# Kernel tuning notes

Measured on AMD Instinct MI355X. Metric: run time of the kernel, lower is better.

Reference implementation:

```python
import jax, jax.numpy as jnp
import numpy as np
from jax import lax

CL, IL = 128, 64            # context_length, inst_length (globals in original)
PC, CH1, CH2, CH3 = 64, 128, 256, 256
CK1 = CK2 = CK3 = 3
F1, OUT = 400, 1
B = 4096
C3_OUT = CH3 * (CL - 1 - CK1 - CK2 - CK3 + 3)   # 256*121 = 30976
F1_IN = C3_OUT + CL * IL                        # 39168


def _uni(k, shape, fan_in):
    s = 1.0 / np.sqrt(fan_in)
    return jax.random.uniform(k, shape, jnp.float32, -s, s)


def setup_inputs() -> dict:
    key = jax.random.key(0)
    ks = jax.random.split(key, 14)
    x = jax.random.normal(ks[0], (B, CL * IL), jnp.float32)
    Wp = _uni(ks[1], (PC, IL, 2), IL * 2); bp = _uni(ks[2], (PC,), IL * 2)
    W1 = _uni(ks[3], (CH1, PC, CK1), PC * CK1); b1 = _uni(ks[4], (CH1,), PC * CK1)
    W2 = _uni(ks[5], (CH2, CH1, CK2), CH1 * CK2); b2 = _uni(ks[6], (CH2,), CH1 * CK2)
    W3 = _uni(ks[7], (CH3, CH2, CK3), CH2 * CK3); b3 = _uni(ks[8], (CH3,), CH2 * CK3)
    Wf1 = _uni(ks[9], (F1, F1_IN), F1_IN); bf1 = _uni(ks[10], (F1,), F1_IN)
    Wf2 = _uni(ks[11], (OUT, F1), F1); bf2 = _uni(ks[12], (OUT,), F1)
    return dict(x=x, Wp=Wp, bp=bp, W1=W1, b1=b1, W2=W2, b2=b2,
                W3=W3, b3=b3, Wf1=Wf1, bf1=bf1, Wf2=Wf2, bf2=bf2)


def _conv1d(h, w, b):
    # h: [B,C,L], w: [O,C,K], valid conv, stride 1
    return lax.conv_general_dilated(h, w, (1,), 'VALID',
                                    dimension_numbers=('NCH', 'OIH', 'NCH')) + b[None, :, None]


def reference(x, Wp, bp, W1, b1, W2, b2, W3, b3, Wf1, bf1, Wf2, bf2):
    b = x.shape[0]
    xt = x.reshape(b, CL, IL).transpose(0, 2, 1)          # [B, IL, CL]
    # Fused pairwise convp: original loops i=1..CL-1 over k=2 Conv1d on
    # (x[:,:,0], x[:,:,i]); equivalent to one shared term + one batched matmul.
    base = jnp.einsum('pc,bc->bp', Wp[:, :, 0], xt[:, :, 0])        # [B, PC]
    rest = jnp.einsum('pc,bci->bpi', Wp[:, :, 1], xt[:, :, 1:])     # [B, PC, CL-1]
    h = jax.nn.relu(base[:, :, None] + rest + bp[None, :, None])
    h = jax.nn.relu(_conv1d(h, W1, b1))
    h = jax.nn.relu(_conv1d(h, W2, b2))
    h = jax.nn.relu(_conv1d(h, W3, b3))
    h = h.reshape(b, C3_OUT)
    h = jnp.concatenate([h, xt.reshape(b, IL * CL)], axis=1)        # [B, F1_IN]
    h = jax.nn.relu(h @ Wf1.T + bf1)
    return h @ Wf2.T + bf2
```

## Files before the change

### kernel.cpp

```cpp
#include <hip/hip_runtime.h>


typedef __attribute__((ext_vector_type(8))) short bf16x8;
typedef __attribute__((ext_vector_type(4))) float f32x4;
typedef __attribute__((ext_vector_type(8))) unsigned short u16x8;
typedef __attribute__((ext_vector_type(4))) unsigned short u16x4;
typedef __attribute__((ext_vector_type(2))) unsigned int u32x2;
typedef __attribute__((ext_vector_type(4))) unsigned int u32x4;

#define DEVINL __device__ __forceinline__

DEVINL unsigned short f2bf(float f) {
  unsigned u = __builtin_bit_cast(unsigned, f);
  return (unsigned short)((u + 0x7fffu + ((u >> 16) & 1u)) >> 16);
}
DEVINL float bf2f(unsigned short h) {
  return __builtin_bit_cast(float, ((unsigned)h) << 16);
}
DEVINL unsigned cvtpk(float lo, float hi) {
  unsigned r;
  asm("v_cvt_pk_bf16_f32 %0, %1, %2" : "=v"(r) : "v"(lo), "v"(hi));
  return r;
}
DEVINL f32x4 mfma16(bf16x8 a, bf16x8 b, f32x4 c) {
  return __builtin_amdgcn_mfma_f32_16x16x32_bf16(a, b, c, 0, 0, 0);
}
DEVINL float relu(float v) { return v > 0.f ? v : 0.f; }
DEVINL int sxg(int r, int c, int sh) {
  return (r << sh) + (((c >> 3) ^ (r & 7)) << 3) + (c & 7);
}

constexpr int NB = 4096;

__global__ __launch_bounds__(256) void k_prep_w(
    const float* __restrict__ Wp, const float* __restrict__ W1,
    const float* __restrict__ W2, const float* __restrict__ W3,
    unsigned short* __restrict__ wp1r, unsigned short* __restrict__ wp0r,
    unsigned short* __restrict__ w1p, unsigned short* __restrict__ w2p,
    unsigned short* __restrict__ w3p) {
  int idx = blockIdx.x * 256 + threadIdx.x;
  if (idx < 4096) {
    int p = idx >> 6, i = idx & 63;
    wp1r[p * 64 + i] = f2bf(Wp[(p * 64 + i) * 2 + 1]);
    wp0r[i * 64 + p] = f2bf(Wp[(p * 64 + i) * 2 + 0]);
    return;
  }
  idx -= 4096;
  if (idx < 24576) {
    int f = idx >> 9, l = (idx >> 3) & 63, e = idx & 7;
    int mt = f & 7, t = f >> 3, ks = t & 1, k = t >> 1;
    int o = mt * 16 + (l & 15), c = ks * 32 + (l >> 4) * 8 + e;
    w1p[idx] = f2bf(W1[(o * 64 + c) * 3 + k]);
    return;
  }
  idx -= 24576;
  if (idx < 98304) {
    int f = idx >> 9, l = (idx >> 3) & 63, e = idx & 7;
    int mt = f & 15, t = f >> 4, ks = t & 3, k = t >> 2;
    int o = mt * 16 + (l & 15), c = ks * 32 + (l >> 4) * 8 + e;
    w2p[idx] = f2bf(W2[(o * 128 + c) * 3 + k]);
    return;
  }
  idx -= 98304;
  if (idx < 196608) {
    int f = idx >> 9, l = (idx >> 3) & 63, e = idx & 7;
    int mt = f & 15, t = f >> 4, ks = t & 7, k = t >> 3;
    int o = mt * 16 + (l & 15), c = ks * 32 + (l >> 4) * 8 + e;
    w3p[idx] = f2bf(W3[(o * 256 + c) * 3 + k]);
  }
}

__global__ __launch_bounds__(256) void k_prep_wf1(const float* __restrict__ wf1,
                                                  unsigned short* __restrict__ wf1r) {
  extern __shared__ unsigned short tls[];
  const int m = blockIdx.x / 5, q = blockIdx.x % 5, tid = threadIdx.x;
  unsigned short* dst = wf1r + (size_t)m * 39168;
  if (q < 4) {
    const float* src = wf1 + (size_t)m * 39168 + q * 7744;
    for (int idx = tid; idx < 7744; idx += 256) {
      int o = idx / 121, l = idx - o * 121;
      tls[o * 132 + l] = f2bf(src[idx]);
    }
    __syncthreads();
    for (int idx = tid; idx < 7744; idx += 256) {
      int l = idx >> 6, o = idx & 63;
      dst[l * 256 + q * 64 + o] = tls[o * 132 + l];
    }
  } else {
    const float* src = wf1 + (size_t)m * 39168 + 30976;
    for (int idx = tid; idx < 8192; idx += 256) {
      int il = idx >> 7, cl = idx & 127;
      tls[cl * 66 + il] = f2bf(src[idx]);
    }
    __syncthreads();
    for (int idx = tid; idx < 8192; idx += 256) {
      int cl = idx >> 6, il = idx & 63;
      dst[30976 + idx] = tls[cl * 66 + il];
    }
  }
}

template <int CIN, int COUT, int LIN, int LOUT, int SSHI, int SSHO, bool TOGLB>
DEVINL void conv16(const unsigned short* in_lds,
                   const unsigned short* __restrict__ wpack,
                   const float* __restrict__ bias, unsigned short* out_lds,
                   unsigned short* h3, int b, int lane, int wv) {
  constexpr int KS = CIN / 32;
  constexpr int MT = COUT / 16;
  constexpr int MPW = MT / 4;
  const int lr = lane & 15, lq = lane >> 4;
  const int wm = wv >> 1, wn = wv & 1;
  f32x4 acc[MPW][4];
#pragma unroll
  for (int mi = 0; mi < MPW; ++mi)
#pragma unroll
    for (int ni = 0; ni < 4; ++ni) acc[mi][ni] = (f32x4){0.f, 0.f, 0.f, 0.f};
#pragma unroll
  for (int k = 0; k < 3; ++k)
#pragma unroll
    for (int ks = 0; ks < KS; ++ks) {
      bf16x8 a[MPW];
#pragma unroll
      for (int mi = 0; mi < MPW; ++mi)
        a[mi] = *(const bf16x8*)(wpack +
                                 (((k * KS + ks) * MT + wm * MPW + mi) << 9) +
                                 lane * 8);
      const int col = ks * 32 + lq * 8;
#pragma unroll
      for (int ni = 0; ni < 4; ++ni) {
        int l = (wn * 4 + ni) * 16 + lr + k;
        if (l > LIN - 1) l = LIN - 1;
        bf16x8 bb = *(const bf16x8*)(in_lds + sxg(l, col, SSHI));
#pragma unroll
        for (int mi = 0; mi < MPW; ++mi)
          acc[mi][ni] = mfma16(a[mi], bb, acc[mi][ni]);
      }
    }
#pragma unroll
  for (int mi = 0; mi < MPW; ++mi) {
    const int o0 = (wm * MPW + mi) * 16 + lq * 4;
    const f32x4 bi = *(const f32x4*)(bias + o0);
#pragma unroll
    for (int ni = 0; ni < 4; ++ni) {
      const int l = (wn * 4 + ni) * 16 + lr;
      if (l < LOUT) {
        u32x2 pk;
        pk.x = cvtpk(relu(acc[mi][ni][0] + bi[0]), relu(acc[mi][ni][1] + bi[1]));
        pk.y = cvtpk(relu(acc[mi][ni][2] + bi[2]), relu(acc[mi][ni][3] + bi[3]));
        if constexpr (TOGLB)
          *(u32x2*)(h3 + ((size_t)b * LOUT + l) * COUT + o0) = pk;
        else
          *(u32x2*)(out_lds + sxg(l, o0, SSHO)) = pk;
      }
    }
  }
}

__global__ __launch_bounds__(512, 1) void k_front(
    const float* __restrict__ x, const unsigned short* __restrict__ wp0r,
    const float* __restrict__ bp, const unsigned short* __restrict__ wp1r,
    const unsigned short* __restrict__ w1p, const float* __restrict__ b1,
    const unsigned short* __restrict__ w2p, const float* __restrict__ b2,
    const unsigned short* __restrict__ w3p, const float* __restrict__ b3,
    unsigned short* __restrict__ h3) {
  extern __shared__ unsigned short lds[];
  unsigned short* xs = lds;
  unsigned short* h1s = lds;
  unsigned short* h0s = lds + 16000;
  unsigned short* h2s = lds + 16000;
  __shared__ float pbase[8][64];
  __shared__ float basel[64];
  const int b = blockIdx.x, tid = threadIdx.x;
  const int lane = tid & 63, wv = tid >> 6, lq = lane >> 4, lr = lane & 15;
  const float* xb = x + (size_t)b * 8192;

  for (int idx = tid * 4; idx < 8192; idx += 2048) {
    f32x4 v = *(const f32x4*)(xb + idx);
    int c = idx >> 6, i = idx & 63;
    u32x2 pk;
    pk.x = cvtpk(v[0], v[1]);
    pk.y = cvtpk(v[2], v[3]);
    *(u32x2*)(xs + sxg(c, i, 6)) = pk;
  }
  __syncthreads();

  {
    int p = tid & 63, q = tid >> 6;
    float s = 0.f;
#pragma unroll
    for (int t = 0; t < 8; ++t) {
      int i = q * 8 + t;
      s += bf2f(wp0r[i * 64 + p]) * bf2f(xs[i]);
    }
    pbase[q][p] = s;
  }
  __syncthreads();
  if (tid < 64) {
    float s = bp[tid];
#pragma unroll
    for (int q = 0; q < 8; ++q) s += pbase[q][tid];
    basel[tid] = s;
  }
  __syncthreads();

  {
    const int mt = wv & 3, nh = wv >> 2;
    f32x4 acc[4];
#pragma unroll
    for (int t = 0; t < 4; ++t) acc[t] = (f32x4){0.f, 0.f, 0.f, 0.f};
#pragma unroll
    for (int s = 0; s < 2; ++s) {
      bf16x8 a = *(const bf16x8*)(wp1r + (mt * 16 + lr) * 64 + s * 32 + lq * 8);
#pragma unroll
      for (int t = 0; t < 4; ++t) {
        int j = (nh * 4 + t) * 16 + lr;
        int row = j + 1 > 127 ? 127 : j + 1;
        bf16x8 bb = *(const bf16x8*)(xs + sxg(row, s * 32 + lq * 8, 6));
        acc[t] = mfma16(a, bb, acc[t]);
      }
    }
    const int m0 = mt * 16 + lq * 4;
    f32x4 bl;
#pragma unroll
    for (int r = 0; r < 4; ++r) bl[r] = basel[m0 + r];
#pragma unroll
    for (int t = 0; t < 4; ++t) {
      int j = (nh * 4 + t) * 16 + lr;
      if (j < 127) {
        u32x2 pk;
        pk.x = cvtpk(relu(acc[t][0] + bl[0]), relu(acc[t][1] + bl[1]));
        pk.y = cvtpk(relu(acc[t][2] + bl[2]), relu(acc[t][3] + bl[3]));
        *(u32x2*)(h0s + sxg(j, m0, 6)) = pk;
      }
    }
  }
  __syncthreads();

  conv16<64, 128, 127, 125, 6, 7, false>(h0s, w1p, b1, h1s, nullptr, b, lane, wv);
  __syncthreads();
  conv16<128, 256, 125, 123, 7, 8, false>(h1s, w2p, b2, h2s, nullptr, b, lane, wv);
  __syncthreads();
  conv16<256, 256, 123, 121, 8, 0, true>(h2s, w3p, b3, nullptr, h3, b, lane, wv);
}

__global__ __launch_bounds__(512, 2) void k_fc1(
    const unsigned short* __restrict__ h3, const float* __restrict__ x,
    const unsigned short* __restrict__ wf1r, float* __restrict__ fpart,
    int chunkN, int S) {
  __shared__ unsigned short lB[2][64 * 64];
  const int tid = threadIdx.x;
  const int lane = tid & 63, wv = tid >> 6, lq = lane >> 4, lr = lane & 15;
  const int slice = blockIdx.x % S;
  const int bbase = (blockIdx.x / S) * 64;
  const int per = 612 / S, rem = 612 % S;
  const int c0 = slice * per + (slice < rem ? slice : rem);
  const int c1 = c0 + per + (slice < rem ? 1 : 0);

  f32x4 acc[3][4], acc24;
#pragma unroll
  for (int mi = 0; mi < 3; ++mi)
#pragma unroll
    for (int nt = 0; nt < 4; ++nt) acc[mi][nt] = (f32x4){0.f, 0.f, 0.f, 0.f};
  acc24 = (f32x4){0.f, 0.f, 0.f, 0.f};

  const size_t arow0 = (size_t)((3 * wv + 0) * 16 + lr) * 39168;
  const size_t arow1 = (size_t)((3 * wv + 1) * 16 + lr) * 39168;
  const size_t arow2 = (size_t)((3 * wv + 2) * 16 + lr) * 39168;
  const size_t arow24 = (size_t)(384 + lr) * 39168;

  const int sn = tid >> 3, sch = tid & 7;
  const unsigned short* hrow = h3 + (size_t)(bbase + sn) * 30976 + sch * 8;
  const float* xrow = x + (size_t)(bbase + sn) * 8192 + sch * 8;
  const int woff = (sn << 6) + ((sch ^ (sn & 7)) << 3);

  u32x4 hv;
  f32x4 xv0, xv1;
  bool isx;

#define FC1_GLOAD(KC)                                                     \
  {                                                                       \
    const int k0_ = (KC)*64;                                              \
    isx = (k0_ >= 30976);                                                 \
    if (!isx) {                                                           \
      hv = *(const u32x4*)(hrow + k0_);                                   \
    } else {                                                              \
      xv0 = *(const f32x4*)(xrow + (k0_ - 30976));                        \
      xv1 = *(const f32x4*)(xrow + (k0_ - 30976) + 4);                    \
    }                                                                     \
  }
#define FC1_DSWRITE(BUF)                                                  \
  {                                                                       \
    if (isx) {                                                            \
      hv.x = cvtpk(xv0[0], xv0[1]);                                       \
      hv.y = cvtpk(xv0[2], xv0[3]);                                       \
      hv.z = cvtpk(xv1[0], xv1[1]);                                       \
      hv.w = cvtpk(xv1[2], xv1[3]);                                       \
    }                                                                     \
    *(u32x4*)(lB[BUF] + woff) = hv;                                       \
  }

  FC1_GLOAD(c0)
  FC1_DSWRITE(0)
  __syncthreads();

  for (int kc = c0; kc < c1; ++kc) {
    const int p = (kc - c0) & 1;
    const int k0 = kc * 64;
    const bool more = (kc + 1 < c1);
    if (more) FC1_GLOAD(kc + 1)

#pragma unroll
    for (int win = 0; win < 2; ++win) {
      const int koff = k0 + win * 32 + lq * 8;
      bf16x8 a0 = *(const bf16x8*)(wf1r + arow0 + koff);
      bf16x8 a1 = *(const bf16x8*)(wf1r + arow1 + koff);
      bf16x8 a2 = *(const bf16x8*)(wf1r + arow2 + koff);
      const int cloc = win * 32 + lq * 8;
#pragma unroll
      for (int nt = 0; nt < 4; ++nt) {
        const int n = nt * 16 + lr;
        bf16x8 bb = *(const bf16x8*)(lB[p] + sxg(n, cloc, 6));
        acc[0][nt] = mfma16(a0, bb, acc[0][nt]);
        acc[1][nt] = mfma16(a1, bb, acc[1][nt]);
        acc[2][nt] = mfma16(a2, bb, acc[2][nt]);
      }
      if (wv < 4) {
        bf16x8 a24 = *(const bf16x8*)(wf1r + arow24 + koff);
        const int n = wv * 16 + lr;
        bf16x8 bb = *(const bf16x8*)(lB[p] + sxg(n, cloc, 6));
        acc24 = mfma16(a24, bb, acc24);
      }
    }
    if (more) FC1_DSWRITE(p ^ 1)
    __syncthreads();
  }
#undef FC1_GLOAD
#undef FC1_DSWRITE

#pragma unroll
  for (int mi = 0; mi < 3; ++mi) {
    const int m0 = (3 * wv + mi) * 16 + lq * 4;
#pragma unroll
    for (int nt = 0; nt < 4; ++nt) {
      const int bb = bbase + nt * 16 + lr;
      *(f32x4*)(fpart + ((size_t)slice * chunkN + bb) * 400 + m0) = acc[mi][nt];
    }
  }
  if (wv < 4) {
    const int bb = bbase + wv * 16 + lr;
    *(f32x4*)(fpart + ((size_t)slice * chunkN + bb) * 400 + 384 + lq * 4) = acc24;
  }
}

__global__ __launch_bounds__(256) void k_fc1red(const float* __restrict__ fpart,
                                                const float* __restrict__ bf1,
                                                float* __restrict__ fc,
                                                int chunkN, int S) {
  int idx = blockIdx.x * 256 + threadIdx.x;
  if (idx >= chunkN * 400) return;
  int m = idx % 400;
  float s = bf1[m];
  size_t stride = (size_t)chunkN * 400;
#pragma unroll 4
  for (int sl = 0; sl < S; ++sl) s += fpart[(size_t)sl * stride + idx];
  fc[idx] = relu(s);
}

__global__ __launch_bounds__(256) void k_fc2(const float* __restrict__ fc,
                                             const float* __restrict__ wf2,
                                             const float* __restrict__ bf2,
                                             float* __restrict__ out) {
  int b = blockIdx.x * 4 + (threadIdx.x >> 6);
  int lane = threadIdx.x & 63;
  float s = 0.f;
  for (int m = lane; m < 400; m += 64) s += fc[(size_t)b * 400 + m] * wf2[m];
#pragma unroll
  for (int off = 32; off > 0; off >>= 1) s += __shfl_down(s, off, 64);
  if (lane == 0) out[b] = s + bf2[0];
}

extern "C" void kernel_launch(void* const* d_in, const int* in_sizes, int n_in,
                              void* d_out, int out_size, void* d_ws, size_t ws_size,
                              hipStream_t stream) {
  const float* x = (const float*)d_in[0];
  const float* Wp = (const float*)d_in[1];
  const float* bp = (const float*)d_in[2];
  const float* W1 = (const float*)d_in[3];
  const float* b1 = (const float*)d_in[4];
  const float* W2 = (const float*)d_in[5];
  const float* b2 = (const float*)d_in[6];
  const float* W3 = (const float*)d_in[7];
  const float* b3 = (const float*)d_in[8];
  const float* Wf1 = (const float*)d_in[9];
  const float* bf1 = (const float*)d_in[10];
  const float* Wf2 = (const float*)d_in[11];
  const float* bf2 = (const float*)d_in[12];
  float* out = (float*)d_out;

  const size_t fixed =
      8192 + 8192 + 49152 + 196608 + 393216 + 400ULL * 39168 * 2;
  const int S = 16;
  static const int cand[3] = {2048, 1024, 512};
  int chunkN = 512;
  for (int i = 0; i < 3; ++i) {
    size_t cn = cand[i];
    size_t need = fixed + cn * 61952ULL + (size_t)S * cn * 1600ULL + cn * 1600ULL;
    if (need <= ws_size) {
      chunkN = cand[i];
      break;
    }
  }
  const int nchunk = NB / chunkN;

  char* ws = (char*)d_ws;
  size_t off = 0;
  unsigned short* h3c = (unsigned short*)(ws + off);
  off += (size_t)chunkN * 61952ULL;
  float* fpart = (float*)(ws + off);
  off += (size_t)S * chunkN * 1600ULL;
  float* fc = (float*)(ws + off);
  off += (size_t)chunkN * 1600ULL;
  unsigned short* wp1r = (unsigned short*)(ws + off);
  off += 8192;
  unsigned short* wp0r = (unsigned short*)(ws + off);
  off += 8192;
  unsigned short* w1p = (unsigned short*)(ws + off);
  off += 49152;
  unsigned short* w2p = (unsigned short*)(ws + off);
  off += 196608;
  unsigned short* w3p = (unsigned short*)(ws + off);
  off += 393216;
  unsigned short* wf1r = (unsigned short*)(ws + off);

  k_prep_w<<<1264, 256, 0, stream>>>(Wp, W1, W2, W3, wp1r, wp0r, w1p, w2p, w3p);
  k_prep_wf1<<<2000, 256, 16896, stream>>>(Wf1, wf1r);

  for (int c = 0; c < nchunk; ++c) {
    const float* xc = x + (size_t)c * chunkN * 8192;
    k_front<<<chunkN, 512, 94976, stream>>>(xc, wp0r, bp, wp1r, w1p, b1, w2p,
                                            b2, w3p, b3, h3c);
    k_fc1<<<(chunkN / 64) * S, 512, 0, stream>>>(h3c, xc, wf1r, fpart, chunkN, S);
    k_fc1red<<<(chunkN * 400 + 255) / 256, 256, 0, stream>>>(fpart, bf1, fc,
                                                             chunkN, S);
    k_fc2<<<chunkN / 4, 256, 0, stream>>>(fc, Wf2, bf2, out + (size_t)c * chunkN);
  }
}
```

Measured before the change: 717.9 us.

## Use 1024-thread blocks for front conv and fc1 with reshaped wave tiling

Doubles the block size of the fused front convolution kernel and the fc1 GEMM kernel to 16 waves and redistributes the per-wave tiles: conv waves now each own 4 M-tiles across a 2D wave grid, and fc1 handles 128 batch rows per block with each wave computing 13 M-tiles over a zero-padded 416-row weight matrix. The intent is to raise the number of waves per CU and amortize LDS B-tile loads across more output rows. In exchange fc1 now reads the A operand straight from global memory for every M-tile of every wave, wastes work on the padded rows, and puts register pressure on 1024-thread blocks.

```diff
diff --git a/kernel.cpp b/kernel.cpp
--- a/kernel.cpp
+++ b/kernel.cpp
@@ -75,6 +75,14 @@
   extern __shared__ unsigned short tls[];
   const int m = blockIdx.x / 5, q = blockIdx.x % 5, tid = threadIdx.x;
   unsigned short* dst = wf1r + (size_t)m * 39168;
+  if (m >= 400) {
+    if (q < 4) {
+      for (int idx = tid; idx < 7744; idx += 256) dst[(idx >> 6) * 256 + q * 64 + (idx & 63)] = 0;
+    } else {
+      for (int idx = tid; idx < 8192; idx += 256) dst[30976 + idx] = 0;
+    }
+    return;
+  }
   if (q < 4) {
     const float* src = wf1 + (size_t)m * 39168 + q * 7744;
     for (int idx = tid; idx < 7744; idx += 256) {
@@ -107,14 +115,18 @@
                    unsigned short* h3, int b, int lane, int wv) {
   constexpr int KS = CIN / 32;
   constexpr int MT = COUT / 16;
-  constexpr int MPW = MT / 4;
+  constexpr int MPW = 4;
+  constexpr int GM = MT / MPW;
+  constexpr int GN = 16 / GM;
+  constexpr int NPW = 8 / GN;
+  static_assert(GM * GN == 16 && GN * NPW == 8, "");
   const int lr = lane & 15, lq = lane >> 4;
-  const int wm = wv >> 1, wn = wv & 1;
-  f32x4 acc[MPW][4];
+  const int wm = wv / GN, wn = wv % GN;
+  f32x4 acc[MPW][NPW];
 #pragma unroll
   for (int mi = 0; mi < MPW; ++mi)
 #pragma unroll
-    for (int ni = 0; ni < 4; ++ni) acc[mi][ni] = (f32x4){0.f, 0.f, 0.f, 0.f};
+    for (int ni = 0; ni < NPW; ++ni) acc[mi][ni] = (f32x4){0.f, 0.f, 0.f, 0.f};
 #pragma unroll
   for (int k = 0; k < 3; ++k)
 #pragma unroll
@@ -127,8 +139,8 @@
                                  lane * 8);
       const int col = ks * 32 + lq * 8;
 #pragma unroll
-      for (int ni = 0; ni < 4; ++ni) {
-        int l = (wn * 4 + ni) * 16 + lr + k;
+      for (int ni = 0; ni < NPW; ++ni) {
+        int l = (wn * NPW + ni) * 16 + lr + k;
         if (l > LIN - 1) l = LIN - 1;
         bf16x8 bb = *(const bf16x8*)(in_lds + sxg(l, col, SSHI));
 #pragma unroll
@@ -141,8 +153,8 @@
     const int o0 = (wm * MPW + mi) * 16 + lq * 4;
     const f32x4 bi = *(const f32x4*)(bias + o0);
 #pragma unroll
-    for (int ni = 0; ni < 4; ++ni) {
-      const int l = (wn * 4 + ni) * 16 + lr;
+    for (int ni = 0; ni < NPW; ++ni) {
+      const int l = (wn * NPW + ni) * 16 + lr;
       if (l < LOUT) {
         u32x2 pk;
         pk.x = cvtpk(relu(acc[mi][ni][0] + bi[0]), relu(acc[mi][ni][1] + bi[1]));
@@ -156,7 +168,7 @@
   }
 }
 
-__global__ __launch_bounds__(512, 1) void k_front(
+__global__ __launch_bounds__(1024) void k_front(
     const float* __restrict__ x, const unsigned short* __restrict__ wp0r,
     const float* __restrict__ bp, const unsigned short* __restrict__ wp1r,
     const unsigned short* __restrict__ w1p, const float* __restrict__ b1,
@@ -168,13 +180,13 @@
   unsigned short* h1s = lds;
   unsigned short* h0s = lds + 16000;
   unsigned short* h2s = lds + 16000;
-  __shared__ float pbase[8][64];
+  __shared__ float pbase[16][64];
   __shared__ float basel[64];
   const int b = blockIdx.x, tid = threadIdx.x;
   const int lane = tid & 63, wv = tid >> 6, lq = lane >> 4, lr = lane & 15;
   const float* xb = x + (size_t)b * 8192;
 
-  for (int idx = tid * 4; idx < 8192; idx += 2048) {
+  for (int idx = tid * 4; idx < 8192; idx += 4096) {
     f32x4 v = *(const f32x4*)(xb + idx);
     int c = idx >> 6, i = idx & 63;
     u32x2 pk;
@@ -188,8 +200,8 @@
     int p = tid & 63, q = tid >> 6;
     float s = 0.f;
 #pragma unroll
-    for (int t = 0; t < 8; ++t) {
-      int i = q * 8 + t;
+    for (int t = 0; t < 4; ++t) {
+      int i = q * 4 + t;
       s += bf2f(wp0r[i * 64 + p]) * bf2f(xs[i]);
     }
     pbase[q][p] = s;
@@ -198,22 +210,22 @@
   if (tid < 64) {
     float s = bp[tid];
 #pragma unroll
-    for (int q = 0; q < 8; ++q) s += pbase[q][tid];
+    for (int q = 0; q < 16; ++q) s += pbase[q][tid];
     basel[tid] = s;
   }
   __syncthreads();
 
   {
     const int mt = wv & 3, nh = wv >> 2;
-    f32x4 acc[4];
-#pragma unroll
-    for (int t = 0; t < 4; ++t) acc[t] = (f32x4){0.f, 0.f, 0.f, 0.f};
+    f32x4 acc[2];
+    acc[0] = (f32x4){0.f, 0.f, 0.f, 0.f};
+    acc[1] = (f32x4){0.f, 0.f, 0.f, 0.f};
 #pragma unroll
     for (int s = 0; s < 2; ++s) {
       bf16x8 a = *(const bf16x8*)(wp1r + (mt * 16 + lr) * 64 + s * 32 + lq * 8);
 #pragma unroll
-      for (int t = 0; t < 4; ++t) {
-        int j = (nh * 4 + t) * 16 + lr;
+      for (int t = 0; t < 2; ++t) {
+        int j = (nh * 2 + t) * 16 + lr;
         int row = j + 1 > 127 ? 127 : j + 1;
         bf16x8 bb = *(const bf16x8*)(xs + sxg(row, s * 32 + lq * 8, 6));
         acc[t] = mfma16(a, bb, acc[t]);
@@ -224,8 +236,8 @@
 #pragma unroll
     for (int r = 0; r < 4; ++r) bl[r] = basel[m0 + r];
 #pragma unroll
-    for (int t = 0; t < 4; ++t) {
-      int j = (nh * 4 + t) * 16 + lr;
+    for (int t = 0; t < 2; ++t) {
+      int j = (nh * 2 + t) * 16 + lr;
       if (j < 127) {
         u32x2 pk;
         pk.x = cvtpk(relu(acc[t][0] + bl[0]), relu(acc[t][1] + bl[1]));
@@ -243,30 +255,28 @@
   conv16<256, 256, 123, 121, 8, 0, true>(h2s, w3p, b3, nullptr, h3, b, lane, wv);
 }
 
-__global__ __launch_bounds__(512, 2) void k_fc1(
+__global__ __launch_bounds__(1024) void k_fc1(
     const unsigned short* __restrict__ h3, const float* __restrict__ x,
     const unsigned short* __restrict__ wf1r, float* __restrict__ fpart,
     int chunkN, int S) {
-  __shared__ unsigned short lB[2][64 * 64];
+  __shared__ unsigned short lB[2][128 * 64];
   const int tid = threadIdx.x;
   const int lane = tid & 63, wv = tid >> 6, lq = lane >> 4, lr = lane & 15;
   const int slice = blockIdx.x % S;
-  const int bbase = (blockIdx.x / S) * 64;
+  const int bbase = (blockIdx.x / S) * 128;
   const int per = 612 / S, rem = 612 % S;
   const int c0 = slice * per + (slice < rem ? slice : rem);
   const int c1 = c0 + per + (slice < rem ? 1 : 0);
-
-  f32x4 acc[3][4], acc24;
-#pragma unroll
-  for (int mi = 0; mi < 3; ++mi)
-#pragma unroll
-    for (int nt = 0; nt < 4; ++nt) acc[mi][nt] = (f32x4){0.f, 0.f, 0.f, 0.f};
-  acc24 = (f32x4){0.f, 0.f, 0.f, 0.f};
-
-  const size_t arow0 = (size_t)((3 * wv + 0) * 16 + lr) * 39168;
-  const size_t arow1 = (size_t)((3 * wv + 1) * 16 + lr) * 39168;
-  const size_t arow2 = (size_t)((3 * wv + 2) * 16 + lr) * 39168;
-  const size_t arow24 = (size_t)(384 + lr) * 39168;
+  const int wm = wv >> 3, wn = wv & 7;
+
+  f32x4 acc[13];
+#pragma unroll
+  for (int mt = 0; mt < 13; ++mt) acc[mt] = (f32x4){0.f, 0.f, 0.f, 0.f};
+
+  size_t arow[13];
+#pragma unroll
+  for (int mt = 0; mt < 13; ++mt)
+    arow[mt] = (size_t)(wm * 208 + mt * 16 + lr) * 39168;
 
   const int sn = tid >> 3, sch = tid & 7;
   const unsigned short* hrow = h3 + (size_t)(bbase + sn) * 30976 + sch * 8;
@@ -303,6 +313,7 @@
   FC1_DSWRITE(0)
   __syncthreads();
 
+  const int n = wn * 16 + lr;
   for (int kc = c0; kc < c1; ++kc) {
     const int p = (kc - c0) & 1;
     const int k0 = kc * 64;
@@ -312,23 +323,12 @@
 #pragma unroll
     for (int win = 0; win < 2; ++win) {
       const int koff = k0 + win * 32 + lq * 8;
-      bf16x8 a0 = *(const bf16x8*)(wf1r + arow0 + koff);
-      bf16x8 a1 = *(const bf16x8*)(wf1r + arow1 + koff);
-      bf16x8 a2 = *(const bf16x8*)(wf1r + arow2 + koff);
       const int cloc = win * 32 + lq * 8;
-#pragma unroll
-      for (int nt = 0; nt < 4; ++nt) {
-        const int n = nt * 16 + lr;
-        bf16x8 bb = *(const bf16x8*)(lB[p] + sxg(n, cloc, 6));
-        acc[0][nt] = mfma16(a0, bb, acc[0][nt]);
-        acc[1][nt] = mfma16(a1, bb, acc[1][nt]);
-        acc[2][nt] = mfma16(a2, bb, acc[2][nt]);
-      }
-      if (wv < 4) {
-        bf16x8 a24 = *(const bf16x8*)(wf1r + arow24 + koff);
-        const int n = wv * 16 + lr;
-        bf16x8 bb = *(const bf16x8*)(lB[p] + sxg(n, cloc, 6));
-        acc24 = mfma16(a24, bb, acc24);
+      bf16x8 bb = *(const bf16x8*)(lB[p] + sxg(n, cloc, 6));
+#pragma unroll
+      for (int mt = 0; mt < 13; ++mt) {
+        bf16x8 av = *(const bf16x8*)(wf1r + arow[mt] + koff);
+        acc[mt] = mfma16(av, bb, acc[mt]);
       }
     }
     if (more) FC1_DSWRITE(p ^ 1)
@@ -337,18 +337,12 @@
 #undef FC1_GLOAD
 #undef FC1_DSWRITE
 
-#pragma unroll
-  for (int mi = 0; mi < 3; ++mi) {
-    const int m0 = (3 * wv + mi) * 16 + lq * 4;
-#pragma unroll
-    for (int nt = 0; nt < 4; ++nt) {
-      const int bb = bbase + nt * 16 + lr;
-      *(f32x4*)(fpart + ((size_t)slice * chunkN + bb) * 400 + m0) = acc[mi][nt];
-    }
-  }
-  if (wv < 4) {
-    const int bb = bbase + wv * 16 + lr;
-    *(f32x4*)(fpart + ((size_t)slice * chunkN + bb) * 400 + 384 + lq * 4) = acc24;
+  const int bb = bbase + wn * 16 + lr;
+#pragma unroll
+  for (int mt = 0; mt < 13; ++mt) {
+    const int m0 = wm * 208 + mt * 16 + lq * 4;
+    if (m0 < 400)
+      *(f32x4*)(fpart + ((size_t)slice * chunkN + bb) * 400 + m0) = acc[mt];
   }
 }
 
@@ -398,7 +392,7 @@
   float* out = (float*)d_out;
 
   const size_t fixed =
-      8192 + 8192 + 49152 + 196608 + 393216 + 400ULL * 39168 * 2;
+      8192 + 8192 + 49152 + 196608 + 393216 + 416ULL * 39168 * 2;
   const int S = 16;
   static const int cand[3] = {2048, 1024, 512};
   int chunkN = 512;
@@ -433,13 +427,14 @@
   unsigned short* wf1r = (unsigned short*)(ws + off);
 
   k_prep_w<<<1264, 256, 0, stream>>>(Wp, W1, W2, W3, wp1r, wp0r, w1p, w2p, w3p);
-  k_prep_wf1<<<2000, 256, 16896, stream>>>(Wf1, wf1r);
+  k_prep_wf1<<<416 * 5, 256, 16896, stream>>>(Wf1, wf1r);
 
   for (int c = 0; c < nchunk; ++c) {
     const float* xc = x + (size_t)c * chunkN * 8192;
-    k_front<<<chunkN, 512, 94976, stream>>>(xc, wp0r, bp, wp1r, w1p, b1, w2p,
-                                            b2, w3p, b3, h3c);
-    k_fc1<<<(chunkN / 64) * S, 512, 0, stream>>>(h3c, xc, wf1r, fpart, chunkN, S);
+    k_front<<<chunkN, 1024, 94976, stream>>>(xc, wp0r, bp, wp1r, w1p, b1, w2p,
+                                             b2, w3p, b3, h3c);
+    k_fc1<<<(chunkN / 128) * S, 1024, 0, stream>>>(h3c, xc, wf1r, fpart,
+                                                   chunkN, S);
     k_fc1red<<<(chunkN * 400 + 255) / 256, 256, 0, stream>>>(fpart, bf1, fc,
                                                              chunkN, S);
     k_fc2<<<chunkN / 4, 256, 0, stream>>>(fc, Wf2, bf2, out + (size_t)c * chunkN);
```

Measured after the change: 1.546 ms. +115.3%, slower.
